# Optimization experiments

Measured on AMD Instinct MI355X. Metric: run time of the kernel, lower is better.

## Reference

```python
import jax, jax.numpy as jnp
import numpy as np

B, N, C_IN = 8, 8192, 64
M, K, RADIUS = 1024, 64, 0.2
MLP = [64, 64, 128]


def _fps(pts, m):
    """Iterative farthest point sampling. pts: [N,3] -> [m] int32 indices."""
    n = pts.shape[0]

    def step(carry, _):
        dists, last = carry
        d = jnp.sum((pts - pts[last]) ** 2, axis=-1)          # [N]
        dists = jnp.minimum(dists, d)
        nxt = jnp.argmax(dists).astype(jnp.int32)
        return (dists, nxt), nxt

    init = (jnp.full((n,), 1e10, pts.dtype), jnp.int32(0))
    _, idx = jax.lax.scan(step, init, None, length=m - 1)
    return jnp.concatenate([jnp.zeros((1,), jnp.int32), idx])


def _ball_query(new_xyz, xyz, radius, k):
    """new_xyz: [B,3,M], xyz: [B,3,N] -> [B,M,K] neighbor indices.
    First k points within radius (in index order); padded with first hit."""
    d2 = (jnp.sum(new_xyz ** 2, 1)[:, :, None] + jnp.sum(xyz ** 2, 1)[:, None, :]
          - 2.0 * jnp.einsum('bcm,bcn->bmn', new_xyz, xyz))   # [B,M,N]
    mask = d2 < radius * radius
    # stable argsort of ~mask puts indices of in-radius points first, in order
    order = jnp.argsort(jnp.where(mask, 0, 1).astype(jnp.int32), axis=-1)[..., :k]
    count = jnp.sum(mask, axis=-1)                             # [B,M]
    valid = jnp.arange(k)[None, None, :] < count[..., None]
    return jnp.where(valid, order, order[..., :1])


def _group(x, idx):
    """x: [B,C,N], idx: [B,...] -> [B,C,...] gathered along N."""
    return jax.vmap(lambda a, i: a[:, i])(x, idx)


def _forward(xyz, feature, params):
    # FPS centroid indices (torch runs under no_grad -> stop_gradient)
    pts = jax.lax.stop_gradient(jnp.transpose(xyz, (0, 2, 1)))  # [B,N,3]
    cidx = jax.vmap(lambda p: _fps(p, M))(pts)                  # [B,M]
    new_xyz = _group(xyz, cidx)                                 # [B,3,M]
    nidx = _ball_query(jax.lax.stop_gradient(new_xyz),
                       jax.lax.stop_gradient(xyz), RADIUS, K)   # [B,M,K]
    gxyz = _group(xyz, nidx) - new_xyz[..., None]               # [B,3,M,K]
    x = jnp.concatenate([gxyz, _group(feature, nidx)], axis=1)  # [B,3+C,M,K]
    # SharedMLP: 1x1 conv2d + BN (folded to per-channel scale/bias) + ReLU
    for w, s, b in params:
        x = jax.nn.relu(jnp.einsum('oi,bimk->bomk', w, x)
                        * s[:, None, None] + b[:, None, None])
    return new_xyz, jnp.max(x, axis=3)                          # [B,3,M], [B,128,M]


def setup_inputs() -> dict:
    key = jax.random.key(0)
    ks = jax.random.split(key, 5)
    inp = {
        'xyz': jax.random.normal(ks[0], (B, 3, N), jnp.float32),
        'feature': jax.random.normal(ks[1], (B, C_IN, N), jnp.float32),
    }
    prev = C_IN + 3  # use_xyz=True
    for li, co in enumerate(MLP):
        inp[f'w{li}'] = jax.random.normal(ks[2 + li], (co, prev), jnp.float32) / np.sqrt(prev).astype(np.float32)
        inp[f's{li}'] = jnp.ones((co,), jnp.float32)
        inp[f'b{li}'] = jnp.zeros((co,), jnp.float32)
        prev = co
    return inp


def reference(xyz, feature, w0, s0, b0, w1, s1, b1, w2, s2, b2):
    return _forward(xyz, feature, ((w0, s0, b0), (w1, s1, b1), (w2, s2, b2)))
```

## Files before the change

kernel.cpp:

```cpp
#include <hip/hip_runtime.h>


#define B_ 8
#define N_ 8192
#define M_ 1024
#define K_ 64
#define FTW 68

template <int CTRL>
__device__ __forceinline__ unsigned long long dpp_key(unsigned long long k) {
  int lo = __builtin_amdgcn_update_dpp(0, (int)(unsigned int)k, CTRL, 0xF, 0xF, true);
  int hi = __builtin_amdgcn_update_dpp(0, (int)(unsigned int)(k >> 32), CTRL, 0xF, 0xF, true);
  unsigned long long o = ((unsigned long long)(unsigned int)hi << 32) | (unsigned int)lo;
  return o > k ? o : k;
}

template <int CTRL>
__device__ __forceinline__ float dpp_fmax(float v) {
  int o = __builtin_amdgcn_update_dpp(0, __float_as_int(v), CTRL, 0xF, 0xF, true);
  return fmaxf(v, __int_as_float(o));
}
__device__ __forceinline__ float wave_fmax63(float v) {
  v = dpp_fmax<0xB1>(v);
  v = dpp_fmax<0x4E>(v);
  v = dpp_fmax<0x141>(v);
  v = dpp_fmax<0x140>(v);
  v = dpp_fmax<0x142>(v);
  v = dpp_fmax<0x143>(v);
  return v;
}

__global__ __launch_bounds__(256, 1) void fps_ft_kernel(const float* __restrict__ xyz,
                                                        const float* __restrict__ feat,
                                                        const float* __restrict__ w0,
                                                        float* __restrict__ w0pad,
                                                        float* __restrict__ ft,
                                                        float* __restrict__ nxyz) {
#pragma clang fp contract(off)
  if (blockIdx.x >= 8) {
    if (blockIdx.x == 8) {
      for (int i = threadIdx.x; i < 64 * FTW; i += 256) {
        int o = i / FTW, c = i % FTW;
        w0pad[i] = (c < 67) ? w0[o * 67 + c] : 0.f;
      }
    }
    const int nb = gridDim.x - 8;
    const int total = B_ * N_ * FTW;
    for (int idx = (blockIdx.x - 8) * 256 + threadIdx.x; idx < total; idx += nb * 256) {
      int c = idx % FTW;
      int bn = idx / FTW;
      int n = bn & (N_ - 1);
      int b = bn >> 13;
      float v;
      if (c < 3) v = xyz[(b * 3 + c) * N_ + n];
      else if (c < 67) v = feat[(b * 64 + (c - 3)) * N_ + n];
      else v = 0.f;
      ft[idx] = v;
    }
    return;
  }

  __shared__ float4 pts4[N_];
  __shared__ unsigned long long cand[2][16];
  __shared__ int scidx[M_];
  const int b = blockIdx.x;
  const int t = threadIdx.x;
  const int lane = t & 63;
  const int wid = t >> 6;
  const float* xb = xyz + b * 3 * N_;

  for (int n = t; n < N_; n += 256) {
    pts4[n] = make_float4(xb[n], xb[N_ + n], xb[2 * N_ + n], 0.f);
  }

  const int base = t * 32;
  float px[32], py[32], pz[32], mind[32];
#pragma unroll
  for (int j = 0; j < 32; ++j) {
    px[j] = xb[base + j];
    py[j] = xb[N_ + base + j];
    pz[j] = xb[2 * N_ + base + j];
    mind[j] = 1e10f;
  }
  float xl = xb[0], yl = xb[N_], zl = xb[2 * N_];
  if (t == 0) scidx[0] = 0;
  __syncthreads();

  for (int i = 1; i < M_; ++i) {
    float bestv = -1.f;
    int bl = 0;
#pragma unroll
    for (int j = 0; j < 32; ++j) {
      float dx = __fsub_rn(px[j], xl);
      float dy = __fsub_rn(py[j], yl);
      float dz = __fsub_rn(pz[j], zl);
      float d = __fadd_rn(__fadd_rn(__fmul_rn(dx, dx), __fmul_rn(dy, dy)), __fmul_rn(dz, dz));
      float md = fminf(mind[j], d);
      mind[j] = md;
      if (md > bestv) { bestv = md; bl = j; }
    }
    unsigned long long key =
        ((unsigned long long)__float_as_uint(bestv) << 32) | (unsigned int)(~(base + bl));
    key = dpp_key<0xB1>(key);
    key = dpp_key<0x4E>(key);
    key = dpp_key<0x141>(key);
    key = dpp_key<0x140>(key);
    if ((lane & 15) == 0) cand[i & 1][wid * 4 + (lane >> 4)] = key;
    __syncthreads();
    unsigned long long gk = cand[i & 1][lane & 15];
    gk = dpp_key<0xB1>(gk);
    gk = dpp_key<0x4E>(gk);
    gk = dpp_key<0x141>(gk);
    gk = dpp_key<0x140>(gk);
    const int gi = (int)(~(unsigned int)gk);
    if (t == 0) scidx[i] = gi;
    float4 cc = pts4[gi];
    xl = cc.x; yl = cc.y; zl = cc.z;
  }
  __syncthreads();
  for (int q = t; q < M_; q += 256) {
    int ci = scidx[q];
    float4 c = pts4[ci];
    nxyz[b * 3 * M_ + q] = c.x;
    nxyz[b * 3 * M_ + M_ + q] = c.y;
    nxyz[b * 3 * M_ + 2 * M_ + q] = c.z;
  }
}

__global__ __launch_bounds__(256) void ballq_kernel(const float* __restrict__ xyz,
                                                    const float* __restrict__ nxyz,
                                                    int* __restrict__ nidx) {
  const int lane = threadIdx.x & 63;
  const int g = blockIdx.x * 4 + (threadIdx.x >> 6);
  const int b = g >> 10;
  const int m = g & (M_ - 1);
  const float* xb = xyz + b * 3 * N_;
  const float cx = nxyz[b * 3 * M_ + m];
  const float cy = nxyz[b * 3 * M_ + M_ + m];
  const float cz = nxyz[b * 3 * M_ + 2 * M_ + m];
  const float nc = __fadd_rn(__fadd_rn(__fmul_rn(cx, cx), __fmul_rn(cy, cy)), __fmul_rn(cz, cz));
  int cnt = 0;
  int first = 0;
  int* slot = nidx + (g << 6);
  for (int basei = 0; basei < N_ && cnt < K_; basei += 64) {
    const int n = basei + lane;
    float p_x = xb[n], p_y = xb[N_ + n], p_z = xb[2 * N_ + n];
    float pn = __fadd_rn(__fadd_rn(__fmul_rn(p_x, p_x), __fmul_rn(p_y, p_y)), __fmul_rn(p_z, p_z));
    float dt = __fadd_rn(__fadd_rn(__fmul_rn(cx, p_x), __fmul_rn(cy, p_y)), __fmul_rn(cz, p_z));
    float d2 = __fsub_rn(__fadd_rn(nc, pn), __fmul_rn(2.f, dt));
    bool inr = d2 < 0.04f;
    unsigned long long mk = __ballot(inr);
    if (cnt == 0 && mk != 0ull) first = basei + (__ffsll((long long)mk) - 1);
    int pos = cnt + (int)__popcll(mk & ((1ull << lane) - 1ull));
    if (inr && pos < K_) slot[pos] = n;
    cnt += (int)__popcll(mk);
  }
  if (cnt > K_) cnt = K_;
  if (lane >= cnt) slot[lane] = first;
}

__global__ __launch_bounds__(128, 2) void mlp_t_kernel(
    const float* __restrict__ ft, const float* __restrict__ w0pad,
    const int* __restrict__ nidx, const float* __restrict__ nxyz,
    const float* __restrict__ s0, const float* __restrict__ b0,
    const float* __restrict__ w1, const float* __restrict__ s1, const float* __restrict__ b1,
    const float* __restrict__ w2, const float* __restrict__ s2, const float* __restrict__ b2,
    float* __restrict__ out2) {
  __shared__ float xls[64 * FTW];
  __shared__ float red[2][128];
  const int g = blockIdx.x;
  const int b = g >> 10;
  const int m = g & (M_ - 1);
  const int t = threadIdx.x;
  const int lane = t & 63;
  const int wid = t >> 6;
  const int r0 = wid * 32;

  const float cx = nxyz[b * 3 * M_ + m];
  const float cy = nxyz[b * 3 * M_ + M_ + m];
  const float cz = nxyz[b * 3 * M_ + 2 * M_ + m];

  {
    const int row = t >> 1;
    const int half = t & 1;
    const int nk = nidx[(g << 6) + row];
    const float4* src = (const float4*)(ft + (size_t)((b << 13) + nk) * FTW);
    float4* dst = (float4*)(xls + row * FTW);
    if (half == 0) {
      float4 v0 = src[0];
      v0.x -= cx; v0.y -= cy; v0.z -= cz;
      dst[0] = v0;
#pragma unroll
      for (int q = 1; q < 8; ++q) dst[q] = src[q];
    } else {
#pragma unroll
      for (int q = 8; q < 17; ++q) dst[q] = src[q];
    }
  }
  __syncthreads();

  float w0r[FTW];
  {
    const float4* wp = (const float4*)(w0pad + lane * FTW);
#pragma unroll
    for (int q = 0; q < 17; ++q) {
      float4 wv = wp[q];
      w0r[4 * q + 0] = wv.x; w0r[4 * q + 1] = wv.y;
      w0r[4 * q + 2] = wv.z; w0r[4 * q + 3] = wv.w;
    }
  }
  const float s0l = s0[lane], b0l = b0[lane];
  for (int kk = 0; kk < 32; kk += 2) {
    const int k = r0 + kk;
    const float4* rowA = (const float4*)(xls + k * FTW);
    const float4* rowB = (const float4*)(xls + (k + 1) * FTW);
    float aA = 0.f, aB = 0.f;
#pragma unroll
    for (int q = 0; q < 17; ++q) {
      float4 xa = rowA[q];
      float4 xbv = rowB[q];
      aA = fmaf(w0r[4 * q + 0], xa.x, aA);
      aA = fmaf(w0r[4 * q + 1], xa.y, aA);
      aA = fmaf(w0r[4 * q + 2], xa.z, aA);
      aA = fmaf(w0r[4 * q + 3], xa.w, aA);
      aB = fmaf(w0r[4 * q + 0], xbv.x, aB);
      aB = fmaf(w0r[4 * q + 1], xbv.y, aB);
      aB = fmaf(w0r[4 * q + 2], xbv.z, aB);
      aB = fmaf(w0r[4 * q + 3], xbv.w, aB);
    }
    xls[k * FTW + lane] = fmaxf(fmaf(aA, s0l, b0l), 0.f);
    xls[(k + 1) * FTW + lane] = fmaxf(fmaf(aB, s0l, b0l), 0.f);
  }

  float w1r[64];
  {
    const float4* wp = (const float4*)(w1 + lane * 64);
#pragma unroll
    for (int q = 0; q < 16; ++q) {
      float4 wv = wp[q];
      w1r[4 * q + 0] = wv.x; w1r[4 * q + 1] = wv.y;
      w1r[4 * q + 2] = wv.z; w1r[4 * q + 3] = wv.w;
    }
  }
  const float s1l = s1[lane], b1l = b1[lane];
  for (int kk = 0; kk < 32; kk += 2) {
    const int k = r0 + kk;
    const float4* rowA = (const float4*)(xls + k * FTW);
    const float4* rowB = (const float4*)(xls + (k + 1) * FTW);
    float aA = 0.f, aB = 0.f;
#pragma unroll
    for (int q = 0; q < 16; ++q) {
      float4 xa = rowA[q];
      float4 xbv = rowB[q];
      aA = fmaf(w1r[4 * q + 0], xa.x, aA);
      aA = fmaf(w1r[4 * q + 1], xa.y, aA);
      aA = fmaf(w1r[4 * q + 2], xa.z, aA);
      aA = fmaf(w1r[4 * q + 3], xa.w, aA);
      aB = fmaf(w1r[4 * q + 0], xbv.x, aB);
      aB = fmaf(w1r[4 * q + 1], xbv.y, aB);
      aB = fmaf(w1r[4 * q + 2], xbv.z, aB);
      aB = fmaf(w1r[4 * q + 3], xbv.w, aB);
    }
    xls[k * FTW + lane] = fmaxf(fmaf(aA, s1l, b1l), 0.f);
    xls[(k + 1) * FTW + lane] = fmaxf(fmaf(aB, s1l, b1l), 0.f);
  }

  float w2a[64], w2b[64];
  {
    const float4* wpa = (const float4*)(w2 + lane * 64);
    const float4* wpb = (const float4*)(w2 + (64 + lane) * 64);
#pragma unroll
    for (int q = 0; q < 16; ++q) {
      float4 wv = wpa[q];
      w2a[4 * q + 0] = wv.x; w2a[4 * q + 1] = wv.y;
      w2a[4 * q + 2] = wv.z; w2a[4 * q + 3] = wv.w;
      float4 wu = wpb[q];
      w2b[4 * q + 0] = wu.x; w2b[4 * q + 1] = wu.y;
      w2b[4 * q + 2] = wu.z; w2b[4 * q + 3] = wu.w;
    }
  }
  const float s2a = s2[lane], b2a = b2[lane];
  const float s2b = s2[64 + lane], b2b = b2[64 + lane];
  float vmaxA = 0.f, vmaxB = 0.f;
  for (int kk = 0; kk < 32; ++kk) {
    const float4* row = (const float4*)(xls + (r0 + kk) * FTW);
    float aA = 0.f, aB = 0.f;
#pragma unroll
    for (int q = 0; q < 16; ++q) {
      float4 xa = row[q];
      aA = fmaf(w2a[4 * q + 0], xa.x, aA);
      aA = fmaf(w2a[4 * q + 1], xa.y, aA);
      aA = fmaf(w2a[4 * q + 2], xa.z, aA);
      aA = fmaf(w2a[4 * q + 3], xa.w, aA);
      aB = fmaf(w2b[4 * q + 0], xa.x, aB);
      aB = fmaf(w2b[4 * q + 1], xa.y, aB);
      aB = fmaf(w2b[4 * q + 2], xa.z, aB);
      aB = fmaf(w2b[4 * q + 3], xa.w, aB);
    }
    vmaxA = fmaxf(vmaxA, fmaxf(fmaf(aA, s2a, b2a), 0.f));
    vmaxB = fmaxf(vmaxB, fmaxf(fmaf(aB, s2b, b2b), 0.f));
  }
  red[wid][lane] = vmaxA;
  red[wid][64 + lane] = vmaxB;
  __syncthreads();
  if (t < 128) {
    float v = fmaxf(red[0][t], red[1][t]);
    out2[(size_t)((b << 7) + t) * M_ + m] = v;
  }
}

__global__ __launch_bounds__(64, 4) void mlp_kernel_fb(
    const float* __restrict__ xyz, const float* __restrict__ feat,
    const int* __restrict__ nidx, const float* __restrict__ nxyz,
    const float* __restrict__ w0, const float* __restrict__ s0, const float* __restrict__ b0,
    const float* __restrict__ w1, const float* __restrict__ s1, const float* __restrict__ b1,
    const float* __restrict__ w2, const float* __restrict__ s2, const float* __restrict__ b2,
    float* __restrict__ out2) {
  __shared__ float ylds[64 * 33];
  const int g = blockIdx.x;
  const int b = g >> 10;
  const int m = g & (M_ - 1);
  const int lane = threadIdx.x;
  const int n = nidx[(g << 6) + lane];
  const float cx = nxyz[b * 3 * M_ + m];
  const float cy = nxyz[b * 3 * M_ + M_ + m];
  const float cz = nxyz[b * 3 * M_ + 2 * M_ + m];

  float x0[67];
  const float* xb = xyz + b * 3 * N_;
  x0[0] = xb[n] - cx; x0[1] = xb[N_ + n] - cy; x0[2] = xb[2 * N_ + n] - cz;
#pragma unroll
  for (int c = 0; c < 64; ++c) x0[3 + c] = feat[((b << 6) + c) * N_ + n];

  float x1[64];
#pragma unroll
  for (int h = 0; h < 2; ++h) {
#pragma unroll 2
    for (int oo = 0; oo < 32; oo += 4) {
      const int o = h * 32 + oo;
      const float* wr = w0 + o * 67;
      float a0 = 0.f, a1 = 0.f, a2 = 0.f, a3 = 0.f;
#pragma unroll
      for (int ci = 0; ci < 67; ++ci) {
        float xvv = x0[ci];
        a0 = fmaf(wr[ci], xvv, a0);
        a1 = fmaf(wr[67 + ci], xvv, a1);
        a2 = fmaf(wr[134 + ci], xvv, a2);
        a3 = fmaf(wr[201 + ci], xvv, a3);
      }
      ylds[lane * 33 + oo + 0] = fmaxf(fmaf(a0, s0[o + 0], b0[o + 0]), 0.f);
      ylds[lane * 33 + oo + 1] = fmaxf(fmaf(a1, s0[o + 1], b0[o + 1]), 0.f);
      ylds[lane * 33 + oo + 2] = fmaxf(fmaf(a2, s0[o + 2], b0[o + 2]), 0.f);
      ylds[lane * 33 + oo + 3] = fmaxf(fmaf(a3, s0[o + 3], b0[o + 3]), 0.f);
    }
#pragma unroll
    for (int c = 0; c < 32; ++c) x1[h * 32 + c] = ylds[lane * 33 + c];
  }

  float x2[64];
#pragma unroll
  for (int h = 0; h < 2; ++h) {
#pragma unroll 2
    for (int oo = 0; oo < 32; oo += 4) {
      const int o = h * 32 + oo;
      const float* wr = w1 + o * 64;
      float a0 = 0.f, a1 = 0.f, a2 = 0.f, a3 = 0.f;
#pragma unroll
      for (int ci = 0; ci < 64; ++ci) {
        float xvv = x1[ci];
        a0 = fmaf(wr[ci], xvv, a0);
        a1 = fmaf(wr[64 + ci], xvv, a1);
        a2 = fmaf(wr[128 + ci], xvv, a2);
        a3 = fmaf(wr[192 + ci], xvv, a3);
      }
      ylds[lane * 33 + oo + 0] = fmaxf(fmaf(a0, s1[o + 0], b1[o + 0]), 0.f);
      ylds[lane * 33 + oo + 1] = fmaxf(fmaf(a1, s1[o + 1], b1[o + 1]), 0.f);
      ylds[lane * 33 + oo + 2] = fmaxf(fmaf(a2, s1[o + 2], b1[o + 2]), 0.f);
      ylds[lane * 33 + oo + 3] = fmaxf(fmaf(a3, s1[o + 3], b1[o + 3]), 0.f);
    }
#pragma unroll
    for (int c = 0; c < 32; ++c) x2[h * 32 + c] = ylds[lane * 33 + c];
  }

  float* outbm = out2 + (size_t)(b * 128) * M_ + m;
#pragma unroll 2
  for (int o = 0; o < 128; o += 4) {
    const float* wr = w2 + o * 64;
    float a0 = 0.f, a1 = 0.f, a2 = 0.f, a3 = 0.f;
#pragma unroll
    for (int ci = 0; ci < 64; ++ci) {
      float xvv = x2[ci];
      a0 = fmaf(wr[ci], xvv, a0);
      a1 = fmaf(wr[64 + ci], xvv, a1);
      a2 = fmaf(wr[128 + ci], xvv, a2);
      a3 = fmaf(wr[192 + ci], xvv, a3);
    }
    float v0 = fmaxf(fmaf(a0, s2[o + 0], b2[o + 0]), 0.f);
    float v1 = fmaxf(fmaf(a1, s2[o + 1], b2[o + 1]), 0.f);
    float v2 = fmaxf(fmaf(a2, s2[o + 2], b2[o + 2]), 0.f);
    float v3 = fmaxf(fmaf(a3, s2[o + 3], b2[o + 3]), 0.f);
    v0 = wave_fmax63(v0);
    v1 = wave_fmax63(v1);
    v2 = wave_fmax63(v2);
    v3 = wave_fmax63(v3);
    float g0 = __int_as_float(__builtin_amdgcn_readlane(__float_as_int(v0), 63));
    float g1 = __int_as_float(__builtin_amdgcn_readlane(__float_as_int(v1), 63));
    float g2 = __int_as_float(__builtin_amdgcn_readlane(__float_as_int(v2), 63));
    float g3 = __int_as_float(__builtin_amdgcn_readlane(__float_as_int(v3), 63));
    if (lane == ((o + 0) & 63)) outbm[(o + 0) * M_] = g0;
    if (lane == ((o + 1) & 63)) outbm[(o + 1) * M_] = g1;
    if (lane == ((o + 2) & 63)) outbm[(o + 2) * M_] = g2;
    if (lane == ((o + 3) & 63)) outbm[(o + 3) * M_] = g3;
  }
}

extern "C" void kernel_launch(void* const* d_in, const int* in_sizes, int n_in,
                              void* d_out, int out_size, void* d_ws, size_t ws_size,
                              hipStream_t stream) {
  const float* xyz = (const float*)d_in[0];
  const float* feat = (const float*)d_in[1];
  const float* w0 = (const float*)d_in[2];
  const float* s0 = (const float*)d_in[3];
  const float* b0 = (const float*)d_in[4];
  const float* w1 = (const float*)d_in[5];
  const float* s1 = (const float*)d_in[6];
  const float* b1 = (const float*)d_in[7];
  const float* w2 = (const float*)d_in[8];
  const float* s2 = (const float*)d_in[9];
  const float* b2 = (const float*)d_in[10];

  float* nxyz = (float*)d_out;
  float* out2 = (float*)d_out + B_ * 3 * M_;

  const size_t nidx_bytes = (size_t)B_ * M_ * K_ * sizeof(int);
  const size_t w0p_bytes = (size_t)64 * FTW * sizeof(float);
  const size_t ft_bytes = (size_t)B_ * N_ * FTW * sizeof(float);
  int* nidx = (int*)d_ws;
  float* w0pad = (float*)((char*)d_ws + nidx_bytes);
  float* ft = (float*)((char*)d_ws + nidx_bytes + w0p_bytes);
  const bool use_ft = ws_size >= nidx_bytes + w0p_bytes + ft_bytes;

  hipLaunchKernelGGL(fps_ft_kernel, dim3(use_ft ? 64 : 8), dim3(256), 0, stream,
                     xyz, feat, w0, w0pad, ft, nxyz);
  hipLaunchKernelGGL(ballq_kernel, dim3(B_ * M_ / 4), dim3(256), 0, stream, xyz, nxyz, nidx);
  if (use_ft) {
    hipLaunchKernelGGL(mlp_t_kernel, dim3(B_ * M_), dim3(128), 0, stream,
                       ft, w0pad, nidx, nxyz, s0, b0, w1, s1, b1, w2, s2, b2, out2);
  } else {
    hipLaunchKernelGGL(mlp_kernel_fb, dim3(B_ * M_), dim3(64), 0, stream,
                       xyz, feat, nidx, nxyz, w0, s0, b0, w1, s1, b1, w2, s2, b2, out2);
  }
}
```

Baseline: 1.223 ms.

## Split FPS in halves and overlap second half with fused ball-query+MLP work

FPS is split into two launches, with the running min-distance state and last index saved to workspace between them. The second FPS half runs in the same kernel as ball-query and MLP work blocks for the first 512 centroids, so the serial FPS tail overlaps with compute. The remaining centroids are handled by a separate work kernel. Ball query is fused into the MLP task, which removes the nidx round trip through global memory. The costs are extra state save/restore, a larger shared-memory union that lowers occupancy of the fused work blocks, and a dependence on FPS blocks being scheduled alongside the work blocks.

```diff
diff --git a/kernel.cpp b/kernel.cpp
--- a/kernel.cpp
+++ b/kernel.cpp
@@ -30,14 +30,281 @@
   return v;
 }
 
-__global__ __launch_bounds__(256, 1) void fps_ft_kernel(const float* __restrict__ xyz,
-                                                        const float* __restrict__ feat,
-                                                        const float* __restrict__ w0,
-                                                        float* __restrict__ w0pad,
-                                                        float* __restrict__ ft,
-                                                        float* __restrict__ nxyz) {
+struct FpsShared {
+  float4 pts4[N_];
+  unsigned long long cand[2][16];
+};
+struct WorkShared {
+  float xls[2][64 * FTW];
+  int islot[2][64];
+  float red[2][2][128];
+};
+union SMemU {
+  FpsShared f;
+  WorkShared w;
+};
+
+__device__ void fps_run(const float* __restrict__ xb, float* __restrict__ nxyz_b,
+                        float* __restrict__ mind_save, int* __restrict__ last_save,
+                        FpsShared& S, int i_begin, int i_end, bool first, int t) {
 #pragma clang fp contract(off)
+  const int lane = t & 63;
+  const int wid = t >> 6;
+
+  for (int n = t; n < N_; n += 256) {
+    S.pts4[n] = make_float4(xb[n], xb[N_ + n], xb[2 * N_ + n], 0.f);
+  }
+
+  const int base = t * 32;
+  float px[32], py[32], pz[32], mind[32];
+#pragma unroll
+  for (int j = 0; j < 32; ++j) {
+    px[j] = xb[base + j];
+    py[j] = xb[N_ + base + j];
+    pz[j] = xb[2 * N_ + base + j];
+  }
+  if (first) {
+#pragma unroll
+    for (int j = 0; j < 32; ++j) mind[j] = 1e10f;
+  } else {
+    const float4* ms = (const float4*)(mind_save + base);
+#pragma unroll
+    for (int q = 0; q < 8; ++q) {
+      float4 v = ms[q];
+      mind[4 * q + 0] = v.x; mind[4 * q + 1] = v.y;
+      mind[4 * q + 2] = v.z; mind[4 * q + 3] = v.w;
+    }
+  }
+  float xl = 0.f, yl = 0.f, zl = 0.f;
+  if (first) {
+    xl = xb[0]; yl = xb[N_]; zl = xb[2 * N_];
+    if (t == 0) { nxyz_b[0] = xl; nxyz_b[M_] = yl; nxyz_b[2 * M_] = zl; }
+  }
+  __syncthreads();
+  if (!first) {
+    const int lg = *last_save;
+    float4 c = S.pts4[lg];
+    xl = c.x; yl = c.y; zl = c.z;
+  }
+
+  int lastg = 0;
+  for (int i = i_begin; i < i_end; ++i) {
+    float bestv = -1.f;
+    int bl = 0;
+#pragma unroll
+    for (int j = 0; j < 32; ++j) {
+      float dx = __fsub_rn(px[j], xl);
+      float dy = __fsub_rn(py[j], yl);
+      float dz = __fsub_rn(pz[j], zl);
+      float d = __fadd_rn(__fadd_rn(__fmul_rn(dx, dx), __fmul_rn(dy, dy)), __fmul_rn(dz, dz));
+      float md = fminf(mind[j], d);
+      mind[j] = md;
+      if (md > bestv) { bestv = md; bl = j; }
+    }
+    unsigned long long key =
+        ((unsigned long long)__float_as_uint(bestv) << 32) | (unsigned int)(~(base + bl));
+    key = dpp_key<0xB1>(key);
+    key = dpp_key<0x4E>(key);
+    key = dpp_key<0x141>(key);
+    key = dpp_key<0x140>(key);
+    if ((lane & 15) == 0) S.cand[i & 1][wid * 4 + (lane >> 4)] = key;
+    __syncthreads();
+    unsigned long long gk = S.cand[i & 1][lane & 15];
+    gk = dpp_key<0xB1>(gk);
+    gk = dpp_key<0x4E>(gk);
+    gk = dpp_key<0x141>(gk);
+    gk = dpp_key<0x140>(gk);
+    const int gi = (int)(~(unsigned int)gk);
+    float4 cc = S.pts4[gi];
+    if (t == 0) { nxyz_b[i] = cc.x; nxyz_b[M_ + i] = cc.y; nxyz_b[2 * M_ + i] = cc.z; }
+    xl = cc.x; yl = cc.y; zl = cc.z;
+    lastg = gi;
+  }
+
+  if (i_end < M_ && mind_save) {
+    float4* ms = (float4*)(mind_save + base);
+#pragma unroll
+    for (int q = 0; q < 8; ++q)
+      ms[q] = make_float4(mind[4 * q + 0], mind[4 * q + 1], mind[4 * q + 2], mind[4 * q + 3]);
+    if (t == 0) *last_save = lastg;
+  }
+}
+
+__device__ void work_task(
+    int b, int m, int t128,
+    float* __restrict__ xls, int* __restrict__ islot, float (*__restrict__ red)[128],
+    const float* __restrict__ xyz, const float* __restrict__ ft,
+    const float* __restrict__ w0pad, const float* __restrict__ nxyz,
+    const float* __restrict__ s0, const float* __restrict__ b0,
+    const float* __restrict__ w1, const float* __restrict__ s1, const float* __restrict__ b1,
+    const float* __restrict__ w2, const float* __restrict__ s2, const float* __restrict__ b2,
+    float* __restrict__ out2) {
+  const int lane = t128 & 63;
+  const int w = t128 >> 6;
+  const float cx = nxyz[b * 3 * M_ + m];
+  const float cy = nxyz[b * 3 * M_ + M_ + m];
+  const float cz = nxyz[b * 3 * M_ + 2 * M_ + m];
+
+  if (w == 0) {
+    const float* xb = xyz + b * 3 * N_;
+    const float nc = __fadd_rn(__fadd_rn(__fmul_rn(cx, cx), __fmul_rn(cy, cy)), __fmul_rn(cz, cz));
+    int cnt = 0;
+    int first = 0;
+    for (int basei = 0; basei < N_ && cnt < K_; basei += 64) {
+      const int n = basei + lane;
+      float p_x = xb[n], p_y = xb[N_ + n], p_z = xb[2 * N_ + n];
+      float pn = __fadd_rn(__fadd_rn(__fmul_rn(p_x, p_x), __fmul_rn(p_y, p_y)), __fmul_rn(p_z, p_z));
+      float dt = __fadd_rn(__fadd_rn(__fmul_rn(cx, p_x), __fmul_rn(cy, p_y)), __fmul_rn(cz, p_z));
+      float d2 = __fsub_rn(__fadd_rn(nc, pn), __fmul_rn(2.f, dt));
+      bool inr = d2 < 0.04f;
+      unsigned long long mk = __ballot(inr);
+      if (cnt == 0 && mk != 0ull) first = basei + (__ffsll((long long)mk) - 1);
+      int pos = cnt + (int)__popcll(mk & ((1ull << lane) - 1ull));
+      if (inr && pos < K_) islot[pos] = n;
+      cnt += (int)__popcll(mk);
+    }
+    if (cnt > K_) cnt = K_;
+    if (lane >= cnt) islot[lane] = first;
+  }
+  __syncthreads();
+
+  {
+    const int row = t128 >> 1;
+    const int half = t128 & 1;
+    const int nk = islot[row];
+    const float4* src = (const float4*)(ft + (size_t)((b << 13) + nk) * FTW);
+    float4* dst = (float4*)(xls + row * FTW);
+    if (half == 0) {
+      float4 v0 = src[0];
+      v0.x -= cx; v0.y -= cy; v0.z -= cz;
+      dst[0] = v0;
+#pragma unroll
+      for (int q = 1; q < 8; ++q) dst[q] = src[q];
+    } else {
+#pragma unroll
+      for (int q = 8; q < 17; ++q) dst[q] = src[q];
+    }
+  }
+  __syncthreads();
+
+  const int r0 = w * 32;
+
+  float w0r[FTW];
+  {
+    const float4* wp = (const float4*)(w0pad + lane * FTW);
+#pragma unroll
+    for (int q = 0; q < 17; ++q) {
+      float4 wv = wp[q];
+      w0r[4 * q + 0] = wv.x; w0r[4 * q + 1] = wv.y;
+      w0r[4 * q + 2] = wv.z; w0r[4 * q + 3] = wv.w;
+    }
+  }
+  const float s0l = s0[lane], b0l = b0[lane];
+  for (int kk = 0; kk < 32; kk += 2) {
+    const int k = r0 + kk;
+    const float4* rowA = (const float4*)(xls + k * FTW);
+    const float4* rowB = (const float4*)(xls + (k + 1) * FTW);
+    float aA = 0.f, aB = 0.f;
+#pragma unroll
+    for (int q = 0; q < 17; ++q) {
+      float4 xa = rowA[q];
+      float4 xbv = rowB[q];
+      aA = fmaf(w0r[4 * q + 0], xa.x, aA);
+      aA = fmaf(w0r[4 * q + 1], xa.y, aA);
+      aA = fmaf(w0r[4 * q + 2], xa.z, aA);
+      aA = fmaf(w0r[4 * q + 3], xa.w, aA);
+      aB = fmaf(w0r[4 * q + 0], xbv.x, aB);
+      aB = fmaf(w0r[4 * q + 1], xbv.y, aB);
+      aB = fmaf(w0r[4 * q + 2], xbv.z, aB);
+      aB = fmaf(w0r[4 * q + 3], xbv.w, aB);
+    }
+    xls[k * FTW + lane] = fmaxf(fmaf(aA, s0l, b0l), 0.f);
+    xls[(k + 1) * FTW + lane] = fmaxf(fmaf(aB, s0l, b0l), 0.f);
+  }
+
+  float w1r[64];
+  {
+    const float4* wp = (const float4*)(w1 + lane * 64);
+#pragma unroll
+    for (int q = 0; q < 16; ++q) {
+      float4 wv = wp[q];
+      w1r[4 * q + 0] = wv.x; w1r[4 * q + 1] = wv.y;
+      w1r[4 * q + 2] = wv.z; w1r[4 * q + 3] = wv.w;
+    }
+  }
+  const float s1l = s1[lane], b1l = b1[lane];
+  for (int kk = 0; kk < 32; kk += 2) {
+    const int k = r0 + kk;
+    const float4* rowA = (const float4*)(xls + k * FTW);
+    const float4* rowB = (const float4*)(xls + (k + 1) * FTW);
+    float aA = 0.f, aB = 0.f;
+#pragma unroll
+    for (int q = 0; q < 16; ++q) {
+      float4 xa = rowA[q];
+      float4 xbv = rowB[q];
+      aA = fmaf(w1r[4 * q + 0], xa.x, aA);
+      aA = fmaf(w1r[4 * q + 1], xa.y, aA);
+      aA = fmaf(w1r[4 * q + 2], xa.z, aA);
+      aA = fmaf(w1r[4 * q + 3], xa.w, aA);
+      aB = fmaf(w1r[4 * q + 0], xbv.x, aB);
+      aB = fmaf(w1r[4 * q + 1], xbv.y, aB);
+      aB = fmaf(w1r[4 * q + 2], xbv.z, aB);
+      aB = fmaf(w1r[4 * q + 3], xbv.w, aB);
+    }
+    xls[k * FTW + lane] = fmaxf(fmaf(aA, s1l, b1l), 0.f);
+    xls[(k + 1) * FTW + lane] = fmaxf(fmaf(aB, s1l, b1l), 0.f);
+  }
+
+  float w2a[64], w2b[64];
+  {
+    const float4* wpa = (const float4*)(w2 + lane * 64);
+    const float4* wpb = (const float4*)(w2 + (64 + lane) * 64);
+#pragma unroll
+    for (int q = 0; q < 16; ++q) {
+      float4 wv = wpa[q];
+      w2a[4 * q + 0] = wv.x; w2a[4 * q + 1] = wv.y;
+      w2a[4 * q + 2] = wv.z; w2a[4 * q + 3] = wv.w;
+      float4 wu = wpb[q];
+      w2b[4 * q + 0] = wu.x; w2b[4 * q + 1] = wu.y;
+      w2b[4 * q + 2] = wu.z; w2b[4 * q + 3] = wu.w;
+    }
+  }
+  const float s2a = s2[lane], b2a = b2[lane];
+  const float s2b = s2[64 + lane], b2b = b2[64 + lane];
+  float vmaxA = 0.f, vmaxB = 0.f;
+  for (int kk = 0; kk < 32; ++kk) {
+    const float4* row = (const float4*)(xls + (r0 + kk) * FTW);
+    float aA = 0.f, aB = 0.f;
+#pragma unroll
+    for (int q = 0; q < 16; ++q) {
+      float4 xa = row[q];
+      aA = fmaf(w2a[4 * q + 0], xa.x, aA);
+      aA = fmaf(w2a[4 * q + 1], xa.y, aA);
+      aA = fmaf(w2a[4 * q + 2], xa.z, aA);
+      aA = fmaf(w2a[4 * q + 3], xa.w, aA);
+      aB = fmaf(w2b[4 * q + 0], xa.x, aB);
+      aB = fmaf(w2b[4 * q + 1], xa.y, aB);
+      aB = fmaf(w2b[4 * q + 2], xa.z, aB);
+      aB = fmaf(w2b[4 * q + 3], xa.w, aB);
+    }
+    vmaxA = fmaxf(vmaxA, fmaxf(fmaf(aA, s2a, b2a), 0.f));
+    vmaxB = fmaxf(vmaxB, fmaxf(fmaf(aB, s2b, b2b), 0.f));
+  }
+  red[w][lane] = vmaxA;
+  red[w][64 + lane] = vmaxB;
+  __syncthreads();
+  float v = fmaxf(red[0][t128], red[1][t128]);
+  out2[(size_t)((b << 7) + t128) * M_ + m] = v;
+}
+
+__global__ __launch_bounds__(256, 1) void fps_build_kernel(
+    const float* __restrict__ xyz, const float* __restrict__ feat,
+    const float* __restrict__ w0, float* __restrict__ w0pad, float* __restrict__ ft,
+    float* __restrict__ nxyz, float* __restrict__ mindws, int* __restrict__ lastws,
+    int i_begin, int i_end, int first, int builders) {
+  __shared__ FpsShared sf;
   if (blockIdx.x >= 8) {
+    if (!builders) return;
     if (blockIdx.x == 8) {
       for (int i = threadIdx.x; i < 64 * FTW; i += 256) {
         int o = i / FTW, c = i % FTW;
@@ -59,72 +326,52 @@
     }
     return;
   }
-
-  __shared__ float4 pts4[N_];
-  __shared__ unsigned long long cand[2][16];
-  __shared__ int scidx[M_];
   const int b = blockIdx.x;
-  const int t = threadIdx.x;
-  const int lane = t & 63;
-  const int wid = t >> 6;
-  const float* xb = xyz + b * 3 * N_;
-
-  for (int n = t; n < N_; n += 256) {
-    pts4[n] = make_float4(xb[n], xb[N_ + n], xb[2 * N_ + n], 0.f);
-  }
-
-  const int base = t * 32;
-  float px[32], py[32], pz[32], mind[32];
-#pragma unroll
-  for (int j = 0; j < 32; ++j) {
-    px[j] = xb[base + j];
-    py[j] = xb[N_ + base + j];
-    pz[j] = xb[2 * N_ + base + j];
-    mind[j] = 1e10f;
-  }
-  float xl = xb[0], yl = xb[N_], zl = xb[2 * N_];
-  if (t == 0) scidx[0] = 0;
-  __syncthreads();
-
-  for (int i = 1; i < M_; ++i) {
-    float bestv = -1.f;
-    int bl = 0;
-#pragma unroll
-    for (int j = 0; j < 32; ++j) {
-      float dx = __fsub_rn(px[j], xl);
-      float dy = __fsub_rn(py[j], yl);
-      float dz = __fsub_rn(pz[j], zl);
-      float d = __fadd_rn(__fadd_rn(__fmul_rn(dx, dx), __fmul_rn(dy, dy)), __fmul_rn(dz, dz));
-      float md = fminf(mind[j], d);
-      mind[j] = md;
-      if (md > bestv) { bestv = md; bl = j; }
-    }
-    unsigned long long key =
-        ((unsigned long long)__float_as_uint(bestv) << 32) | (unsigned int)(~(base + bl));
-    key = dpp_key<0xB1>(key);
-    key = dpp_key<0x4E>(key);
-    key = dpp_key<0x141>(key);
-    key = dpp_key<0x140>(key);
-    if ((lane & 15) == 0) cand[i & 1][wid * 4 + (lane >> 4)] = key;
-    __syncthreads();
-    unsigned long long gk = cand[i & 1][lane & 15];
-    gk = dpp_key<0xB1>(gk);
-    gk = dpp_key<0x4E>(gk);
-    gk = dpp_key<0x141>(gk);
-    gk = dpp_key<0x140>(gk);
-    const int gi = (int)(~(unsigned int)gk);
-    if (t == 0) scidx[i] = gi;
-    float4 cc = pts4[gi];
-    xl = cc.x; yl = cc.y; zl = cc.z;
-  }
-  __syncthreads();
-  for (int q = t; q < M_; q += 256) {
-    int ci = scidx[q];
-    float4 c = pts4[ci];
-    nxyz[b * 3 * M_ + q] = c.x;
-    nxyz[b * 3 * M_ + M_ + q] = c.y;
-    nxyz[b * 3 * M_ + 2 * M_ + q] = c.z;
-  }
+  fps_run(xyz + b * 3 * N_, nxyz + b * 3 * M_,
+          mindws ? mindws + (b << 13) : nullptr, lastws ? lastws + b : nullptr,
+          sf, i_begin, i_end, first != 0, threadIdx.x);
+}
+
+__global__ __launch_bounds__(256, 1) void fps_work_kernel(
+    const float* __restrict__ xyz, const float* __restrict__ ft,
+    const float* __restrict__ w0pad, float* __restrict__ nxyz,
+    float* __restrict__ mindws, int* __restrict__ lastws,
+    const float* __restrict__ s0, const float* __restrict__ b0,
+    const float* __restrict__ w1, const float* __restrict__ s1, const float* __restrict__ b1,
+    const float* __restrict__ w2, const float* __restrict__ s2, const float* __restrict__ b2,
+    float* __restrict__ out2) {
+  __shared__ SMemU s;
+  if (blockIdx.x < 8) {
+    const int b = blockIdx.x;
+    fps_run(xyz + b * 3 * N_, nxyz + b * 3 * M_, mindws + (b << 13), lastws + b,
+            s.f, 512, 1024, false, threadIdx.x);
+    return;
+  }
+  const int pair = blockIdx.x - 8;
+  const int tg = threadIdx.x >> 7;
+  const int t128 = threadIdx.x & 127;
+  const int task = pair * 2 + tg;
+  const int b = task >> 9;
+  const int m = task & 511;
+  work_task(b, m, t128, s.w.xls[tg], s.w.islot[tg], s.w.red[tg],
+            xyz, ft, w0pad, nxyz, s0, b0, w1, s1, b1, w2, s2, b2, out2);
+}
+
+__global__ __launch_bounds__(128, 2) void work_kernel(
+    const float* __restrict__ xyz, const float* __restrict__ ft,
+    const float* __restrict__ w0pad, const float* __restrict__ nxyz,
+    const float* __restrict__ s0, const float* __restrict__ b0,
+    const float* __restrict__ w1, const float* __restrict__ s1, const float* __restrict__ b1,
+    const float* __restrict__ w2, const float* __restrict__ s2, const float* __restrict__ b2,
+    float* __restrict__ out2, int m_off) {
+  __shared__ float xls[64 * FTW];
+  __shared__ int islot[64];
+  __shared__ float red[2][128];
+  const int task = blockIdx.x;
+  const int b = task >> 9;
+  const int m = m_off + (task & 511);
+  work_task(b, m, threadIdx.x, xls, islot, red,
+            xyz, ft, w0pad, nxyz, s0, b0, w1, s1, b1, w2, s2, b2, out2);
 }
 
 __global__ __launch_bounds__(256) void ballq_kernel(const float* __restrict__ xyz,
@@ -159,156 +406,6 @@
   if (lane >= cnt) slot[lane] = first;
 }
 
-__global__ __launch_bounds__(128, 2) void mlp_t_kernel(
-    const float* __restrict__ ft, const float* __restrict__ w0pad,
-    const int* __restrict__ nidx, const float* __restrict__ nxyz,
-    const float* __restrict__ s0, const float* __restrict__ b0,
-    const float* __restrict__ w1, const float* __restrict__ s1, const float* __restrict__ b1,
-    const float* __restrict__ w2, const float* __restrict__ s2, const float* __restrict__ b2,
-    float* __restrict__ out2) {
-  __shared__ float xls[64 * FTW];
-  __shared__ float red[2][128];
-  const int g = blockIdx.x;
-  const int b = g >> 10;
-  const int m = g & (M_ - 1);
-  const int t = threadIdx.x;
-  const int lane = t & 63;
-  const int wid = t >> 6;
-  const int r0 = wid * 32;
-
-  const float cx = nxyz[b * 3 * M_ + m];
-  const float cy = nxyz[b * 3 * M_ + M_ + m];
-  const float cz = nxyz[b * 3 * M_ + 2 * M_ + m];
-
-  {
-    const int row = t >> 1;
-    const int half = t & 1;
-    const int nk = nidx[(g << 6) + row];
-    const float4* src = (const float4*)(ft + (size_t)((b << 13) + nk) * FTW);
-    float4* dst = (float4*)(xls + row * FTW);
-    if (half == 0) {
-      float4 v0 = src[0];
-      v0.x -= cx; v0.y -= cy; v0.z -= cz;
-      dst[0] = v0;
-#pragma unroll
-      for (int q = 1; q < 8; ++q) dst[q] = src[q];
-    } else {
-#pragma unroll
-      for (int q = 8; q < 17; ++q) dst[q] = src[q];
-    }
-  }
-  __syncthreads();
-
-  float w0r[FTW];
-  {
-    const float4* wp = (const float4*)(w0pad + lane * FTW);
-#pragma unroll
-    for (int q = 0; q < 17; ++q) {
-      float4 wv = wp[q];
-      w0r[4 * q + 0] = wv.x; w0r[4 * q + 1] = wv.y;
-      w0r[4 * q + 2] = wv.z; w0r[4 * q + 3] = wv.w;
-    }
-  }
-  const float s0l = s0[lane], b0l = b0[lane];
-  for (int kk = 0; kk < 32; kk += 2) {
-    const int k = r0 + kk;
-    const float4* rowA = (const float4*)(xls + k * FTW);
-    const float4* rowB = (const float4*)(xls + (k + 1) * FTW);
-    float aA = 0.f, aB = 0.f;
-#pragma unroll
-    for (int q = 0; q < 17; ++q) {
-      float4 xa = rowA[q];
-      float4 xbv = rowB[q];
-      aA = fmaf(w0r[4 * q + 0], xa.x, aA);
-      aA = fmaf(w0r[4 * q + 1], xa.y, aA);
-      aA = fmaf(w0r[4 * q + 2], xa.z, aA);
-      aA = fmaf(w0r[4 * q + 3], xa.w, aA);
-      aB = fmaf(w0r[4 * q + 0], xbv.x, aB);
-      aB = fmaf(w0r[4 * q + 1], xbv.y, aB);
-      aB = fmaf(w0r[4 * q + 2], xbv.z, aB);
-      aB = fmaf(w0r[4 * q + 3], xbv.w, aB);
-    }
-    xls[k * FTW + lane] = fmaxf(fmaf(aA, s0l, b0l), 0.f);
-    xls[(k + 1) * FTW + lane] = fmaxf(fmaf(aB, s0l, b0l), 0.f);
-  }
-
-  float w1r[64];
-  {
-    const float4* wp = (const float4*)(w1 + lane * 64);
-#pragma unroll
-    for (int q = 0; q < 16; ++q) {
-      float4 wv = wp[q];
-      w1r[4 * q + 0] = wv.x; w1r[4 * q + 1] = wv.y;
-      w1r[4 * q + 2] = wv.z; w1r[4 * q + 3] = wv.w;
-    }
-  }
-  const float s1l = s1[lane], b1l = b1[lane];
-  for (int kk = 0; kk < 32; kk += 2) {
-    const int k = r0 + kk;
-    const float4* rowA = (const float4*)(xls + k * FTW);
-    const float4* rowB = (const float4*)(xls + (k + 1) * FTW);
-    float aA = 0.f, aB = 0.f;
-#pragma unroll
-    for (int q = 0; q < 16; ++q) {
-      float4 xa = rowA[q];
-      float4 xbv = rowB[q];
-      aA = fmaf(w1r[4 * q + 0], xa.x, aA);
-      aA = fmaf(w1r[4 * q + 1], xa.y, aA);
-      aA = fmaf(w1r[4 * q + 2], xa.z, aA);
-      aA = fmaf(w1r[4 * q + 3], xa.w, aA);
-      aB = fmaf(w1r[4 * q + 0], xbv.x, aB);
-      aB = fmaf(w1r[4 * q + 1], xbv.y, aB);
-      aB = fmaf(w1r[4 * q + 2], xbv.z, aB);
-      aB = fmaf(w1r[4 * q + 3], xbv.w, aB);
-    }
-    xls[k * FTW + lane] = fmaxf(fmaf(aA, s1l, b1l), 0.f);
-    xls[(k + 1) * FTW + lane] = fmaxf(fmaf(aB, s1l, b1l), 0.f);
-  }
-
-  float w2a[64], w2b[64];
-  {
-    const float4* wpa = (const float4*)(w2 + lane * 64);
-    const float4* wpb = (const float4*)(w2 + (64 + lane) * 64);
-#pragma unroll
-    for (int q = 0; q < 16; ++q) {
-      float4 wv = wpa[q];
-      w2a[4 * q + 0] = wv.x; w2a[4 * q + 1] = wv.y;
-      w2a[4 * q + 2] = wv.z; w2a[4 * q + 3] = wv.w;
-      float4 wu = wpb[q];
-      w2b[4 * q + 0] = wu.x; w2b[4 * q + 1] = wu.y;
-      w2b[4 * q + 2] = wu.z; w2b[4 * q + 3] = wu.w;
-    }
-  }
-  const float s2a = s2[lane], b2a = b2[lane];
-  const float s2b = s2[64 + lane], b2b = b2[64 + lane];
-  float vmaxA = 0.f, vmaxB = 0.f;
-  for (int kk = 0; kk < 32; ++kk) {
-    const float4* row = (const float4*)(xls + (r0 + kk) * FTW);
-    float aA = 0.f, aB = 0.f;
-#pragma unroll
-    for (int q = 0; q < 16; ++q) {
-      float4 xa = row[q];
-      aA = fmaf(w2a[4 * q + 0], xa.x, aA);
-      aA = fmaf(w2a[4 * q + 1], xa.y, aA);
-      aA = fmaf(w2a[4 * q + 2], xa.z, aA);
-      aA = fmaf(w2a[4 * q + 3], xa.w, aA);
-      aB = fmaf(w2b[4 * q + 0], xa.x, aB);
-      aB = fmaf(w2b[4 * q + 1], xa.y, aB);
-      aB = fmaf(w2b[4 * q + 2], xa.z, aB);
-      aB = fmaf(w2b[4 * q + 3], xa.w, aB);
-    }
-    vmaxA = fmaxf(vmaxA, fmaxf(fmaf(aA, s2a, b2a), 0.f));
-    vmaxB = fmaxf(vmaxB, fmaxf(fmaf(aB, s2b, b2b), 0.f));
-  }
-  red[wid][lane] = vmaxA;
-  red[wid][64 + lane] = vmaxB;
-  __syncthreads();
-  if (t < 128) {
-    float v = fmaxf(red[0][t], red[1][t]);
-    out2[(size_t)((b << 7) + t) * M_ + m] = v;
-  }
-}
-
 __global__ __launch_bounds__(64, 4) void mlp_kernel_fb(
     const float* __restrict__ xyz, const float* __restrict__ feat,
     const int* __restrict__ nidx, const float* __restrict__ nxyz,
@@ -432,21 +529,30 @@
   float* nxyz = (float*)d_out;
   float* out2 = (float*)d_out + B_ * 3 * M_;
 
-  const size_t nidx_bytes = (size_t)B_ * M_ * K_ * sizeof(int);
-  const size_t w0p_bytes = (size_t)64 * FTW * sizeof(float);
+  const size_t w0p_off = 0;
+  const size_t mind_off = 17408;
+  const size_t last_off = mind_off + (size_t)B_ * 8192 * sizeof(float);
+  const size_t ft_off = last_off + 32;
   const size_t ft_bytes = (size_t)B_ * N_ * FTW * sizeof(float);
-  int* nidx = (int*)d_ws;
-  float* w0pad = (float*)((char*)d_ws + nidx_bytes);
-  float* ft = (float*)((char*)d_ws + nidx_bytes + w0p_bytes);
-  const bool use_ft = ws_size >= nidx_bytes + w0p_bytes + ft_bytes;
-
-  hipLaunchKernelGGL(fps_ft_kernel, dim3(use_ft ? 64 : 8), dim3(256), 0, stream,
-                     xyz, feat, w0, w0pad, ft, nxyz);
-  hipLaunchKernelGGL(ballq_kernel, dim3(B_ * M_ / 4), dim3(256), 0, stream, xyz, nxyz, nidx);
+  float* w0pad = (float*)((char*)d_ws + w0p_off);
+  float* mindws = (float*)((char*)d_ws + mind_off);
+  int* lastws = (int*)((char*)d_ws + last_off);
+  float* ft = (float*)((char*)d_ws + ft_off);
+  const bool use_ft = ws_size >= ft_off + ft_bytes;
+
   if (use_ft) {
-    hipLaunchKernelGGL(mlp_t_kernel, dim3(B_ * M_), dim3(128), 0, stream,
-                       ft, w0pad, nidx, nxyz, s0, b0, w1, s1, b1, w2, s2, b2, out2);
+    hipLaunchKernelGGL(fps_build_kernel, dim3(64), dim3(256), 0, stream,
+                       xyz, feat, w0, w0pad, ft, nxyz, mindws, lastws, 1, 512, 1, 1);
+    hipLaunchKernelGGL(fps_work_kernel, dim3(8 + 2048), dim3(256), 0, stream,
+                       xyz, ft, w0pad, nxyz, mindws, lastws,
+                       s0, b0, w1, s1, b1, w2, s2, b2, out2);
+    hipLaunchKernelGGL(work_kernel, dim3(4096), dim3(128), 0, stream,
+                       xyz, ft, w0pad, nxyz, s0, b0, w1, s1, b1, w2, s2, b2, out2, 512);
   } else {
+    int* nidx = (int*)d_ws;
+    hipLaunchKernelGGL(fps_build_kernel, dim3(8), dim3(256), 0, stream,
+                       xyz, feat, w0, nullptr, nullptr, nxyz, nullptr, nullptr, 1, 1024, 1, 0);
+    hipLaunchKernelGGL(ballq_kernel, dim3(B_ * M_ / 4), dim3(256), 0, stream, xyz, nxyz, nidx);
     hipLaunchKernelGGL(mlp_kernel_fb, dim3(B_ * M_), dim3(64), 0, stream,
                        xyz, feat, nidx, nxyz, w0, s0, b0, w1, s1, b1, w2, s2, b2, out2);
   }
```

After: 2.294 ms. +87.6%, slower.

## Split layer-3 MLP channels across waves to cut registers and raise occupancy

Applied to the files above, without the earlier changes.

Reassigns the final MLP layer so each wave computes 64 output channels over all 64 neighbours instead of 128 channels over half the neighbours. This halves the per-thread weight register array and removes the cross-wave shared-memory max reduction. Launch bounds are raised to allow four blocks per CU. It adds a block barrier, and each wave now reads all rows from LDS, which doubles LDS read traffic.

```diff
diff --git a/kernel.cpp b/kernel.cpp
--- a/kernel.cpp
+++ b/kernel.cpp
@@ -159,7 +159,7 @@
   if (lane >= cnt) slot[lane] = first;
 }
 
-__global__ __launch_bounds__(128, 2) void mlp_t_kernel(
+__global__ __launch_bounds__(128, 4) void mlp_t_kernel(
     const float* __restrict__ ft, const float* __restrict__ w0pad,
     const int* __restrict__ nidx, const float* __restrict__ nxyz,
     const float* __restrict__ s0, const float* __restrict__ b0,
@@ -167,7 +167,6 @@
     const float* __restrict__ w2, const float* __restrict__ s2, const float* __restrict__ b2,
     float* __restrict__ out2) {
   __shared__ float xls[64 * FTW];
-  __shared__ float red[2][128];
   const int g = blockIdx.x;
   const int b = g >> 10;
   const int m = g & (M_ - 1);
@@ -264,49 +263,42 @@
     xls[k * FTW + lane] = fmaxf(fmaf(aA, s1l, b1l), 0.f);
     xls[(k + 1) * FTW + lane] = fmaxf(fmaf(aB, s1l, b1l), 0.f);
   }
-
-  float w2a[64], w2b[64];
+  __syncthreads();
+
+  const int ch = (wid << 6) + lane;
+  float w2r[64];
   {
-    const float4* wpa = (const float4*)(w2 + lane * 64);
-    const float4* wpb = (const float4*)(w2 + (64 + lane) * 64);
+    const float4* wp = (const float4*)(w2 + ch * 64);
 #pragma unroll
     for (int q = 0; q < 16; ++q) {
-      float4 wv = wpa[q];
-      w2a[4 * q + 0] = wv.x; w2a[4 * q + 1] = wv.y;
-      w2a[4 * q + 2] = wv.z; w2a[4 * q + 3] = wv.w;
-      float4 wu = wpb[q];
-      w2b[4 * q + 0] = wu.x; w2b[4 * q + 1] = wu.y;
-      w2b[4 * q + 2] = wu.z; w2b[4 * q + 3] = wu.w;
-    }
-  }
-  const float s2a = s2[lane], b2a = b2[lane];
-  const float s2b = s2[64 + lane], b2b = b2[64 + lane];
-  float vmaxA = 0.f, vmaxB = 0.f;
-  for (int kk = 0; kk < 32; ++kk) {
-    const float4* row = (const float4*)(xls + (r0 + kk) * FTW);
+      float4 wv = wp[q];
+      w2r[4 * q + 0] = wv.x; w2r[4 * q + 1] = wv.y;
+      w2r[4 * q + 2] = wv.z; w2r[4 * q + 3] = wv.w;
+    }
+  }
+  const float s2c = s2[ch], b2c = b2[ch];
+  float vmax = 0.f;
+  for (int k = 0; k < 64; k += 2) {
+    const float4* rowA = (const float4*)(xls + k * FTW);
+    const float4* rowB = (const float4*)(xls + (k + 1) * FTW);
     float aA = 0.f, aB = 0.f;
 #pragma unroll
     for (int q = 0; q < 16; ++q) {
-      float4 xa = row[q];
-      aA = fmaf(w2a[4 * q + 0], xa.x, aA);
-      aA = fmaf(w2a[4 * q + 1], xa.y, aA);
-      aA = fmaf(w2a[4 * q + 2], xa.z, aA);
-      aA = fmaf(w2a[4 * q + 3], xa.w, aA);
-      aB = fmaf(w2b[4 * q + 0], xa.x, aB);
-      aB = fmaf(w2b[4 * q + 1], xa.y, aB);
-      aB = fmaf(w2b[4 * q + 2], xa.z, aB);
-      aB = fmaf(w2b[4 * q + 3], xa.w, aB);
-    }
-    vmaxA = fmaxf(vmaxA, fmaxf(fmaf(aA, s2a, b2a), 0.f));
-    vmaxB = fmaxf(vmaxB, fmaxf(fmaf(aB, s2b, b2b), 0.f));
-  }
-  red[wid][lane] = vmaxA;
-  red[wid][64 + lane] = vmaxB;
-  __syncthreads();
-  if (t < 128) {
-    float v = fmaxf(red[0][t], red[1][t]);
-    out2[(size_t)((b << 7) + t) * M_ + m] = v;
-  }
+      float4 xa = rowA[q];
+      float4 xbv = rowB[q];
+      aA = fmaf(w2r[4 * q + 0], xa.x, aA);
+      aA = fmaf(w2r[4 * q + 1], xa.y, aA);
+      aA = fmaf(w2r[4 * q + 2], xa.z, aA);
+      aA = fmaf(w2r[4 * q + 3], xa.w, aA);
+      aB = fmaf(w2r[4 * q + 0], xbv.x, aB);
+      aB = fmaf(w2r[4 * q + 1], xbv.y, aB);
+      aB = fmaf(w2r[4 * q + 2], xbv.z, aB);
+      aB = fmaf(w2r[4 * q + 3], xbv.w, aB);
+    }
+    vmax = fmaxf(vmax, fmaxf(fmaf(aA, s2c, b2c), 0.f));
+    vmax = fmaxf(vmax, fmaxf(fmaf(aB, s2c, b2c), 0.f));
+  }
+  out2[(size_t)((b << 7) + ch) * M_ + m] = vmax;
 }
 
 __global__ __launch_bounds__(64, 4) void mlp_kernel_fb(
```

Result: no change. 1.234 ms (+0.9%).
